# Kernel optimization log

Hardware: AMD Instinct MI355X
Metric: run time of the kernel (lower is better)

## Reference

```python
import jax, jax.numpy as jnp
import numpy as np

S, B, H, N = 512, 32, 512, 131072  # seq_len, batch, hidden_dim, num candidate spans
MAX_STEP = 20  # max_length


def setup_inputs() -> dict:
    key = jax.random.key(0)
    ks = jax.random.split(key, 8)
    hidden = jax.random.normal(ks[0], (S, B, 2 * H), dtype=jnp.float32)
    span_bids = jax.random.randint(ks[1], (N,), 0, B, dtype=jnp.int32)
    # begin in [1, S-1-MAX_STEP-1] so that begin-1>=0 and end=begin+step <= S-1
    span_begins = jax.random.randint(ks[2], (N,), 1, S - MAX_STEP - 2, dtype=jnp.int32)
    steps = jax.random.randint(ks[3], (N,), 2, MAX_STEP + 1, dtype=jnp.int32)
    span_ends = span_begins + steps
    span_flags = jax.random.randint(ks[4], (N,), 0, 2, dtype=jnp.int32)
    span_weights = jax.random.uniform(ks[5], (N,), dtype=jnp.float32)
    W1 = jax.random.normal(ks[6], (2 * H, H), dtype=jnp.float32) / np.sqrt(2.0 * H)
    b1 = jnp.zeros((H,), dtype=jnp.float32)
    W2 = jax.random.normal(ks[7], (H, 1), dtype=jnp.float32) / np.sqrt(float(H))
    b2 = jnp.zeros((1,), dtype=jnp.float32)
    return {"hidden": hidden, "span_bids": span_bids, "span_begins": span_begins,
            "span_ends": span_ends, "span_flags": span_flags, "span_weights": span_weights,
            "W1": W1, "b1": b1, "W2": W2, "b2": b2}


def reference(hidden, span_bids, span_begins, span_ends, span_flags, span_weights, W1, b1, W2, b2):
    h = W2.shape[0]  # hidden_dim
    # vectorized _span_embed: fwd diff on first half, bwd diff on second half
    fwd = hidden[span_ends - 1, span_bids, :h] - hidden[span_begins - 1, span_bids, :h]
    bwd = hidden[span_begins, span_bids, h:] - hidden[span_ends, span_bids, h:]
    feats = jnp.concatenate([fwd, bwd], axis=-1)  # [N, 2H]
    z = jnp.maximum(feats @ W1 + b1, 0.0)
    p = jax.nn.sigmoid(z @ W2 + b2)[:, 0]  # [N]
    targets = (span_flags == 1).astype(p.dtype)
    n_pos = jnp.sum(targets)
    n_tot = jnp.asarray(targets.shape[0], p.dtype)
    scale = 2.0 * n_pos / n_tot  # negative weights scaled by 2*P/(P+N)
    w_eff = jnp.where(span_flags == 1, span_weights, span_weights * scale)
    pc = jnp.clip(p, 1e-7, 1.0 - 1e-7)
    bce = -(targets * jnp.log(pc) + (1.0 - targets) * jnp.log(1.0 - pc))
    loss = jnp.mean(w_eff * bce)
    return loss
```

## Files before the change

kernel.cpp:

```cpp
#include <hip/hip_runtime.h>
#include <hip/hip_bf16.h>


typedef float f32x4 __attribute__((ext_vector_type(4)));
typedef float f32x2 __attribute__((ext_vector_type(2)));
typedef __bf16 bf16x8 __attribute__((ext_vector_type(8)));

__device__ __forceinline__ unsigned short f2bf(float f) {
  unsigned int u = __float_as_uint(f);
  u += 0x7fffu + ((u >> 16) & 1u);
  return (unsigned short)(u >> 16);
}
__device__ __forceinline__ float bf2f(unsigned int lo16) {
  return __uint_as_float(lo16 << 16);
}

__global__ void w1_blocked(const float* __restrict__ W1,
                           unsigned short* __restrict__ W1b) {
  int idx = blockIdx.x * 256 + threadIdx.x;
  int kc = idx & 3;
  int n  = (idx >> 2) & 511;
  int c  = idx >> 11;
  int k0 = c * 32 + kc * 8;
  unsigned short tmp[8];
#pragma unroll
  for (int j = 0; j < 8; ++j)
    tmp[j] = f2bf(W1[(k0 + j) * 512 + n]);
  *(uint4*)(W1b + c * 16384 + n * 32 + kc * 8) = *(uint4*)tmp;
}

__global__ void span_hist(const int* __restrict__ bids, int* __restrict__ ghist,
                          int nspans) {
  __shared__ int h[32];
  int t = threadIdx.x;
  if (t < 32) h[t] = 0;
  __syncthreads();
  int base = blockIdx.x * 1024;
#pragma unroll
  for (int i = 0; i < 4; ++i) {
    int idx = base + t + i * 256;
    if (idx < nspans) atomicAdd(&h[bids[idx]], 1);
  }
  __syncthreads();
  if (t < 32) atomicAdd(&ghist[t], h[t]);
}

__global__ void span_scatter(const int* __restrict__ bids,
                             const int* __restrict__ ghist,
                             int* __restrict__ gslot,
                             int* __restrict__ sidx, int nspans) {
  __shared__ int lh[32], lbase[32], lcur[32];
  int t = threadIdx.x;
  if (t < 32) lh[t] = 0;
  __syncthreads();
  int base = blockIdx.x * 512;
  int myb[2];
#pragma unroll
  for (int i = 0; i < 2; ++i) {
    int idx = base + t + i * 256;
    myb[i] = (idx < nspans) ? bids[idx] : -1;
    if (myb[i] >= 0) atomicAdd(&lh[myb[i]], 1);
  }
  __syncthreads();
  if (t < 32) {
    int pre = 0;
    for (int j = 0; j < t; ++j) pre += ghist[j];
    lbase[t] = pre + atomicAdd(&gslot[t], lh[t]);
    lcur[t] = 0;
  }
  __syncthreads();
#pragma unroll
  for (int i = 0; i < 2; ++i) {
    int b = myb[i];
    if (b >= 0) {
      int pos = lbase[b] + atomicAdd(&lcur[b], 1);
      sidx[pos] = base + t + i * 256;
    }
  }
}

#define APITCH 522
__global__ __launch_bounds__(512, 4) void proj_gemm(
    const float* __restrict__ hidden,
    const unsigned short* __restrict__ w1b,
    unsigned char* __restrict__ Wq) {
  __shared__ __align__(16) unsigned short AH[64 * APITCH];
  unsigned short* Eb = AH;

  const int t = threadIdx.x;
  const int lane = t & 63;
  const int w = t >> 6;
  const int r0 = blockIdx.x << 6;
  const int hk = blockIdx.y << 9;
  const int q = lane >> 4;
  const int m = lane & 15;

  {
    const int col = (t & 31) << 4;
    const int rsub = t >> 5;
#pragma unroll
    for (int p = 0; p < 4; ++p) {
      int row = (p << 4) + rsub;
      const float4* gp = (const float4*)(hidden + ((r0 + row) << 10) + hk + col);
      float4 f0 = gp[0], f1 = gp[1], f2 = gp[2], f3 = gp[3];
      bf16x8 va, vb;
      va[0] = (__bf16)f0.x; va[1] = (__bf16)f0.y;
      va[2] = (__bf16)f0.z; va[3] = (__bf16)f0.w;
      va[4] = (__bf16)f1.x; va[5] = (__bf16)f1.y;
      va[6] = (__bf16)f1.z; va[7] = (__bf16)f1.w;
      vb[0] = (__bf16)f2.x; vb[1] = (__bf16)f2.y;
      vb[2] = (__bf16)f2.z; vb[3] = (__bf16)f2.w;
      vb[4] = (__bf16)f3.x; vb[5] = (__bf16)f3.y;
      vb[6] = (__bf16)f3.z; vb[7] = (__bf16)f3.w;
      unsigned short* dst = AH + row * APITCH + col;
      *(bf16x8*)dst = va;
      *(bf16x8*)(dst + 8) = vb;
    }
  }
  __syncthreads();

  int boffn[4];
#pragma unroll
  for (int nt = 0; nt < 4; ++nt)
    boffn[nt] = (((w << 6) + (nt << 4) + m) << 5) + (q << 3);
  const unsigned short* w1base = w1b + (blockIdx.y << 18);

  f32x4 acc[4][4];
#pragma unroll
  for (int i = 0; i < 4; ++i)
#pragma unroll
    for (int j = 0; j < 4; ++j) acc[i][j] = (f32x4){0.f, 0.f, 0.f, 0.f};

#pragma unroll
  for (int it = 0; it < 16; ++it) {
    const unsigned short* bt = w1base + (it << 14);
    bf16x8 bfr[4];
#pragma unroll
    for (int nt = 0; nt < 4; ++nt)
      bfr[nt] = *(const bf16x8*)(bt + boffn[nt]);
    bf16x8 af[4];
#pragma unroll
    for (int mt = 0; mt < 4; ++mt)
      af[mt] = *(const bf16x8*)(AH + ((mt << 4) + m) * APITCH + (it << 5) + (q << 3));
#pragma unroll
    for (int mt = 0; mt < 4; ++mt)
#pragma unroll
      for (int nt = 0; nt < 4; ++nt)
        acc[mt][nt] = __builtin_amdgcn_mfma_f32_16x16x32_bf16(af[mt], bfr[nt],
                                                              acc[mt][nt], 0, 0, 0);
  }
  __syncthreads();

  unsigned short* Ew = Eb + w * (32 * 72);
#pragma unroll
  for (int pass = 0; pass < 2; ++pass) {
#pragma unroll
    for (int mh = 0; mh < 2; ++mh) {
      int mt = (pass << 1) + mh;
#pragma unroll
      for (int r = 0; r < 4; ++r) {
        int rr = (mh << 4) + ((lane >> 4) << 2) + r;
#pragma unroll
        for (int nt = 0; nt < 4; ++nt)
          Ew[rr * 72 + (nt << 4) + m] = f2bf(acc[mt][nt][r]);
      }
    }
#pragma unroll
    for (int i = 0; i < 4; ++i) {
      int task = (i << 6) + lane;
      int rr = task >> 3;
      int ck = task & 7;
      uint4 v = *(const uint4*)&Ew[rr * 72 + (ck << 3)];
      float f0 = bf2f(v.x & 0xffff), f1 = bf2f(v.x >> 16);
      float f2 = bf2f(v.y & 0xffff), f3 = bf2f(v.y >> 16);
      float f4 = bf2f(v.z & 0xffff), f5 = bf2f(v.z >> 16);
      float f6 = bf2f(v.w & 0xffff), f7 = bf2f(v.w >> 16);
      uint2 o;
      o.x = __builtin_amdgcn_cvt_pk_fp8_f32(f0, f1, 0, false);
      o.x = __builtin_amdgcn_cvt_pk_fp8_f32(f2, f3, o.x, true);
      o.y = __builtin_amdgcn_cvt_pk_fp8_f32(f4, f5, 0, false);
      o.y = __builtin_amdgcn_cvt_pk_fp8_f32(f6, f7, o.y, true);
      int grow = r0 + (pass << 5) + rr;
      int col = (w << 6) + (ck << 3);
      if (hk == 0) {
        *(uint2*)(Wq + (grow << 10) + col) = o;
      } else if (grow >= 32) {
        *(uint2*)(Wq + ((grow - 32) << 10) + 512 + col) = o;
      }
    }
  }
}

#define SPB 64
__global__ __launch_bounds__(256) void span_eval(
    const unsigned char* __restrict__ Wq,
    const int* __restrict__ sidx,
    const int* __restrict__ bids, const int* __restrict__ begins,
    const int* __restrict__ ends, const int* __restrict__ flags,
    const float* __restrict__ weights,
    const float* __restrict__ b1, const float* __restrict__ w2,
    const float* __restrict__ b2, float* __restrict__ partials) {
  __shared__ int oB[SPB], oE[SPB], sfl[SPB];
  __shared__ float swt[SPB];
  __shared__ float red[4][3];
  const int t = threadIdx.x;
  const int lane = t & 63;
  const int w = t >> 6;
  const int h = lane >> 5;
  const int hl = lane & 31;

  const int nblk = gridDim.x;
  int lb = blockIdx.x;
  if ((nblk & 7) == 0) {
    const int cpx = nblk >> 3;
    lb = (blockIdx.x & 7) * cpx + (blockIdx.x >> 3);
  }
  const int sbase = lb * SPB;

  if (t < SPB) {
    int s = sidx[sbase + t];
    int b = bids[s], bg = begins[s], en = ends[s];
    oB[t] = (((bg - 1) << 5) + b) << 10;
    oE[t] = (((en - 1) << 5) + b) << 10;
    sfl[t] = flags[s];
    swt[t] = weights[s];
  }
  __syncthreads();

  const int sp0 = ((w << 1) + h) << 3;
  const int c0 = hl << 4;
  float b1v[16], w2v[16];
#pragma unroll
  for (int q = 0; q < 4; ++q) {
    float4 bv = *(const float4*)(b1 + c0 + (q << 2));
    float4 wv = *(const float4*)(w2 + c0 + (q << 2));
    b1v[(q << 2) + 0] = bv.x; b1v[(q << 2) + 1] = bv.y;
    b1v[(q << 2) + 2] = bv.z; b1v[(q << 2) + 3] = bv.w;
    w2v[(q << 2) + 0] = wv.x; w2v[(q << 2) + 1] = wv.y;
    w2v[(q << 2) + 2] = wv.z; w2v[(q << 2) + 3] = wv.w;
  }

  auto dec = [](unsigned int v, float* f) {
    f32x2 a = __builtin_amdgcn_cvt_pk_f32_fp8(v, false);
    f32x2 b = __builtin_amdgcn_cvt_pk_f32_fp8(v, true);
    f[0] = a[0]; f[1] = a[1]; f[2] = b[0]; f[3] = b[1];
  };

  uint4 BU[3], BV[3], EU[3], EV[3];
  auto ld = [&](int slot, int j) {
    int ob = oB[sp0 + j], oe = oE[sp0 + j];
    BU[slot] = *(const uint4*)(Wq + ob + c0);
    BV[slot] = *(const uint4*)(Wq + ob + 512 + c0);
    EU[slot] = *(const uint4*)(Wq + oe + c0);
    EV[slot] = *(const uint4*)(Wq + oe + 512 + c0);
  };
  ld(0, 0); ld(1, 1); ld(2, 2);

  float mylogit = 0.f;
#pragma unroll
  for (int j = 0; j < 8; ++j) {
    const int slot = j % 3;
    float buf[16], bvf[16], euf[16], evf[16];
    dec(BU[slot].x, buf); dec(BU[slot].y, buf + 4);
    dec(BU[slot].z, buf + 8); dec(BU[slot].w, buf + 12);
    dec(BV[slot].x, bvf); dec(BV[slot].y, bvf + 4);
    dec(BV[slot].z, bvf + 8); dec(BV[slot].w, bvf + 12);
    dec(EU[slot].x, euf); dec(EU[slot].y, euf + 4);
    dec(EU[slot].z, euf + 8); dec(EU[slot].w, euf + 12);
    dec(EV[slot].x, evf); dec(EV[slot].y, evf + 4);
    dec(EV[slot].z, evf + 8); dec(EV[slot].w, evf + 12);
    if (j + 3 < 8) ld(slot, j + 3);
    float sv = 0.f;
#pragma unroll
    for (int k = 0; k < 16; ++k) {
      float zp = euf[k] - buf[k] + bvf[k] - evf[k] + b1v[k];
      sv += fmaxf(zp, 0.f) * w2v[k];
    }
    sv += __shfl_xor(sv, 1);
    sv += __shfl_xor(sv, 2);
    sv += __shfl_xor(sv, 4);
    sv += __shfl_xor(sv, 8);
    sv += __shfl_xor(sv, 16);
    if (hl == j) mylogit = sv;
  }

  mylogit = __shfl(mylogit, ((lane & 8) << 2) + (lane & 7));

  float pos_t = 0.f, neg_t = 0.f, cnt_t = 0.f;
  if (lane < 16) {
    int sl = (w << 4) + lane;
    float logit = mylogit + b2[0];
    float p = 1.f / (1.f + expf(-logit));
    p = fminf(fmaxf(p, 1e-7f), 1.f - 1e-7f);
    int fl = sfl[sl];
    float bce = (fl == 1) ? -logf(p) : -logf(1.f - p);
    float term = swt[sl] * bce;
    pos_t = (fl == 1) ? term : 0.f;
    neg_t = (fl == 1) ? 0.f : term;
    cnt_t = (fl == 1) ? 1.f : 0.f;
  }
#pragma unroll
  for (int off = 1; off < 64; off <<= 1) {
    pos_t += __shfl_xor(pos_t, off);
    neg_t += __shfl_xor(neg_t, off);
    cnt_t += __shfl_xor(cnt_t, off);
  }
  if (lane == 0) { red[w][0] = pos_t; red[w][1] = neg_t; red[w][2] = cnt_t; }
  __syncthreads();
  if (t == 0) {
    partials[(blockIdx.x << 2) + 0] = red[0][0] + red[1][0] + red[2][0] + red[3][0];
    partials[(blockIdx.x << 2) + 1] = red[0][1] + red[1][1] + red[2][1] + red[3][1];
    partials[(blockIdx.x << 2) + 2] = red[0][2] + red[1][2] + red[2][2] + red[3][2];
  }
}

__global__ void finalize(const float* __restrict__ parts, int nblk,
                         float* __restrict__ out, int nspans) {
  __shared__ float sp[4], sn[4], sc[4];
  float P = 0.f, Ng = 0.f, C = 0.f;
  for (int i = threadIdx.x; i < nblk; i += 256) {
    P += parts[(i << 2) + 0];
    Ng += parts[(i << 2) + 1];
    C += parts[(i << 2) + 2];
  }
#pragma unroll
  for (int off = 1; off < 64; off <<= 1) {
    P += __shfl_xor(P, off);
    Ng += __shfl_xor(Ng, off);
    C += __shfl_xor(C, off);
  }
  int w = threadIdx.x >> 6;
  if ((threadIdx.x & 63) == 0) { sp[w] = P; sn[w] = Ng; sc[w] = C; }
  __syncthreads();
  if (threadIdx.x == 0) {
    P = sp[0] + sp[1] + sp[2] + sp[3];
    Ng = sn[0] + sn[1] + sn[2] + sn[3];
    C = sc[0] + sc[1] + sc[2] + sc[3];
    float scale = 2.f * C / (float)nspans;
    out[0] = (P + scale * Ng) / (float)nspans;
  }
}

extern "C" void kernel_launch(void* const* d_in, const int* in_sizes, int n_in,
                              void* d_out, int out_size, void* d_ws, size_t ws_size,
                              hipStream_t stream) {
  const float* hidden = (const float*)d_in[0];
  const int* bids     = (const int*)d_in[1];
  const int* begins   = (const int*)d_in[2];
  const int* ends     = (const int*)d_in[3];
  const int* flags    = (const int*)d_in[4];
  const float* weights = (const float*)d_in[5];
  const float* W1 = (const float*)d_in[6];
  const float* b1 = (const float*)d_in[7];
  const float* W2 = (const float*)d_in[8];
  const float* b2 = (const float*)d_in[9];
  float* out = (float*)d_out;
  const int nspans = in_sizes[1];
  const int nblk = nspans / SPB;

  float* partials = (float*)d_ws;
  unsigned short* W1b = (unsigned short*)((char*)d_ws + (1 << 18));
  unsigned char* Wq = (unsigned char*)((char*)d_ws + (2 << 20));
  int* ghist = (int*)((char*)d_ws + (19 << 20));
  int* gslot = ghist + 32;
  int* sidx  = (int*)((char*)d_ws + (20 << 20));

  hipMemsetAsync(ghist, 0, 64 * sizeof(int), stream);
  w1_blocked<<<256, 256, 0, stream>>>(W1, W1b);
  span_hist<<<(nspans + 1023) / 1024, 256, 0, stream>>>(bids, ghist, nspans);
  span_scatter<<<(nspans + 511) / 512, 256, 0, stream>>>(bids, ghist, gslot,
                                                         sidx, nspans);
  proj_gemm<<<dim3(256, 2), 512, 0, stream>>>(hidden, W1b, Wq);
  span_eval<<<nblk, 256, 0, stream>>>(Wq, sidx, bids, begins, ends, flags,
                                      weights, b1, W2, b2, partials);
  finalize<<<1, 256, 0, stream>>>(partials, nblk, out, nspans);
}
```

Before: 172.0 us.

## Merge prep kernels and retile projection GEMM with swizzled double-chunk LDS staging

Fuses the W1 bf16 blocking kernel and the span histogram kernel into one launch, which saves one launch. Restructures the projection GEMM to use 256-thread blocks over a 3D grid that also splits N, so each block covers 256 output columns. The K dimension is staged through a smaller LDS buffer in two chunks with an XOR-swizzled layout to avoid bank conflicts, and s_setprio is raised around the MFMA blocks. This gives more blocks and smaller LDS for occupancy, but each hidden tile is now loaded and converted twice, once per N half.

```diff
diff --git a/kernel.cpp b/kernel.cpp
--- a/kernel.cpp
+++ b/kernel.cpp
@@ -5,6 +5,7 @@
 typedef float f32x4 __attribute__((ext_vector_type(4)));
 typedef float f32x2 __attribute__((ext_vector_type(2)));
 typedef __bf16 bf16x8 __attribute__((ext_vector_type(8)));
+typedef __bf16 bf16x4 __attribute__((ext_vector_type(4)));
 
 __device__ __forceinline__ unsigned short f2bf(float f) {
   unsigned int u = __float_as_uint(f);
@@ -15,34 +16,35 @@
   return __uint_as_float(lo16 << 16);
 }
 
-__global__ void w1_blocked(const float* __restrict__ W1,
-                           unsigned short* __restrict__ W1b) {
-  int idx = blockIdx.x * 256 + threadIdx.x;
-  int kc = idx & 3;
-  int n  = (idx >> 2) & 511;
-  int c  = idx >> 11;
-  int k0 = c * 32 + kc * 8;
-  unsigned short tmp[8];
-#pragma unroll
-  for (int j = 0; j < 8; ++j)
-    tmp[j] = f2bf(W1[(k0 + j) * 512 + n]);
-  *(uint4*)(W1b + c * 16384 + n * 32 + kc * 8) = *(uint4*)tmp;
-}
-
-__global__ void span_hist(const int* __restrict__ bids, int* __restrict__ ghist,
-                          int nspans) {
+__global__ void prep(const float* __restrict__ W1,
+                     unsigned short* __restrict__ W1b,
+                     const int* __restrict__ bids, int* __restrict__ ghist,
+                     int nspans) {
   __shared__ int h[32];
   int t = threadIdx.x;
-  if (t < 32) h[t] = 0;
-  __syncthreads();
-  int base = blockIdx.x * 1024;
-#pragma unroll
-  for (int i = 0; i < 4; ++i) {
-    int idx = base + t + i * 256;
-    if (idx < nspans) atomicAdd(&h[bids[idx]], 1);
-  }
-  __syncthreads();
-  if (t < 32) atomicAdd(&ghist[t], h[t]);
+  if (blockIdx.x < 256) {
+    int idx = blockIdx.x * 256 + t;
+    int kc = idx & 3;
+    int n  = (idx >> 2) & 511;
+    int c  = idx >> 11;
+    int k0 = c * 32 + kc * 8;
+    unsigned short tmp[8];
+#pragma unroll
+    for (int j = 0; j < 8; ++j)
+      tmp[j] = f2bf(W1[(k0 + j) * 512 + n]);
+    *(uint4*)(W1b + c * 16384 + n * 32 + kc * 8) = *(uint4*)tmp;
+  } else {
+    if (t < 32) h[t] = 0;
+    __syncthreads();
+    int base = (blockIdx.x - 256) * 1024;
+#pragma unroll
+    for (int i = 0; i < 4; ++i) {
+      int idx = base + t + i * 256;
+      if (idx < nspans) atomicAdd(&h[bids[idx]], 1);
+    }
+    __syncthreads();
+    if (t < 32) atomicAdd(&ghist[t], h[t]);
+  }
 }
 
 __global__ void span_scatter(const int* __restrict__ bids,
@@ -79,51 +81,27 @@
   }
 }
 
-#define APITCH 522
-__global__ __launch_bounds__(512, 4) void proj_gemm(
+__global__ __launch_bounds__(256, 4) void proj_gemm(
     const float* __restrict__ hidden,
     const unsigned short* __restrict__ w1b,
     unsigned char* __restrict__ Wq) {
-  __shared__ __align__(16) unsigned short AH[64 * APITCH];
-  unsigned short* Eb = AH;
+  __shared__ __align__(16) unsigned short LB[16384];
 
   const int t = threadIdx.x;
   const int lane = t & 63;
   const int w = t >> 6;
-  const int r0 = blockIdx.x << 6;
-  const int hk = blockIdx.y << 9;
   const int q = lane >> 4;
   const int m = lane & 15;
-
-  {
-    const int col = (t & 31) << 4;
-    const int rsub = t >> 5;
-#pragma unroll
-    for (int p = 0; p < 4; ++p) {
-      int row = (p << 4) + rsub;
-      const float4* gp = (const float4*)(hidden + ((r0 + row) << 10) + hk + col);
-      float4 f0 = gp[0], f1 = gp[1], f2 = gp[2], f3 = gp[3];
-      bf16x8 va, vb;
-      va[0] = (__bf16)f0.x; va[1] = (__bf16)f0.y;
-      va[2] = (__bf16)f0.z; va[3] = (__bf16)f0.w;
-      va[4] = (__bf16)f1.x; va[5] = (__bf16)f1.y;
-      va[6] = (__bf16)f1.z; va[7] = (__bf16)f1.w;
-      vb[0] = (__bf16)f2.x; vb[1] = (__bf16)f2.y;
-      vb[2] = (__bf16)f2.z; vb[3] = (__bf16)f2.w;
-      vb[4] = (__bf16)f3.x; vb[5] = (__bf16)f3.y;
-      vb[6] = (__bf16)f3.z; vb[7] = (__bf16)f3.w;
-      unsigned short* dst = AH + row * APITCH + col;
-      *(bf16x8*)dst = va;
-      *(bf16x8*)(dst + 8) = vb;
-    }
-  }
-  __syncthreads();
-
+  const int r0 = blockIdx.x << 6;
+  const int yc = blockIdx.y << 8;
+  const int z  = blockIdx.z;
+  const int hk = z << 9;
+
+  const unsigned short* w1base = w1b + (z << 18);
   int boffn[4];
 #pragma unroll
   for (int nt = 0; nt < 4; ++nt)
-    boffn[nt] = (((w << 6) + (nt << 4) + m) << 5) + (q << 3);
-  const unsigned short* w1base = w1b + (blockIdx.y << 18);
+    boffn[nt] = ((yc + (w << 6) + (nt << 4) + m) << 5) + (q << 3);
 
   f32x4 acc[4][4];
 #pragma unroll
@@ -131,27 +109,56 @@
 #pragma unroll
     for (int j = 0; j < 4; ++j) acc[i][j] = (f32x4){0.f, 0.f, 0.f, 0.f};
 
-#pragma unroll
-  for (int it = 0; it < 16; ++it) {
-    const unsigned short* bt = w1base + (it << 14);
-    bf16x8 bfr[4];
-#pragma unroll
-    for (int nt = 0; nt < 4; ++nt)
-      bfr[nt] = *(const bf16x8*)(bt + boffn[nt]);
-    bf16x8 af[4];
-#pragma unroll
-    for (int mt = 0; mt < 4; ++mt)
-      af[mt] = *(const bf16x8*)(AH + ((mt << 4) + m) * APITCH + (it << 5) + (q << 3));
-#pragma unroll
-    for (int mt = 0; mt < 4; ++mt)
+  const int s_itL = lane >> 3;
+  const int s_q   = (lane >> 1) & 3;
+  const int s_kk0 = (lane & 1) << 2;
+  const int s_perm = ((s_itL << 1) | (s_itL >> 2)) & 15;
+
+#pragma unroll
+  for (int chunk = 0; chunk < 2; ++chunk) {
+    {
+      const int kb = chunk << 8;
+      const float* gbase = hidden + hk + kb + (lane << 2);
+#pragma unroll
+      for (int i = 0; i < 16; ++i) {
+        int row = (w << 4) + i;
+        float4 f = *(const float4*)(gbase + ((r0 + row) << 10));
+        bf16x4 hv;
+        hv[0] = (__bf16)f.x; hv[1] = (__bf16)f.y;
+        hv[2] = (__bf16)f.z; hv[3] = (__bf16)f.w;
+        int slot = (s_q << 4) + i;
+        int sw = slot ^ s_perm;
+        *(bf16x4*)(LB + (((s_itL << 2) + w) << 9) + (sw << 3) + s_kk0) = hv;
+      }
+    }
+    __syncthreads();
+
+#pragma unroll
+    for (int itL = 0; itL < 8; ++itL) {
+      const unsigned short* bt = w1base + (((chunk << 3) + itL) << 14);
+      bf16x8 bfr[4];
 #pragma unroll
       for (int nt = 0; nt < 4; ++nt)
-        acc[mt][nt] = __builtin_amdgcn_mfma_f32_16x16x32_bf16(af[mt], bfr[nt],
-                                                              acc[mt][nt], 0, 0, 0);
-  }
-  __syncthreads();
-
-  unsigned short* Ew = Eb + w * (32 * 72);
+        bfr[nt] = *(const bf16x8*)(bt + boffn[nt]);
+      const int perm = ((itL << 1) | (itL >> 2)) & 15;
+      const int sw = ((q << 4) + m) ^ perm;
+      bf16x8 af[4];
+#pragma unroll
+      for (int mt = 0; mt < 4; ++mt)
+        af[mt] = *(const bf16x8*)(LB + (((itL << 2) + mt) << 9) + (sw << 3));
+      __builtin_amdgcn_s_setprio(1);
+#pragma unroll
+      for (int mt = 0; mt < 4; ++mt)
+#pragma unroll
+        for (int nt = 0; nt < 4; ++nt)
+          acc[mt][nt] = __builtin_amdgcn_mfma_f32_16x16x32_bf16(af[mt], bfr[nt],
+                                                                acc[mt][nt], 0, 0, 0);
+      __builtin_amdgcn_s_setprio(0);
+    }
+    __syncthreads();
+  }
+
+  unsigned short* Ew = LB + w * (32 * 72);
 #pragma unroll
   for (int pass = 0; pass < 2; ++pass) {
 #pragma unroll
@@ -181,8 +188,8 @@
       o.y = __builtin_amdgcn_cvt_pk_fp8_f32(f4, f5, 0, false);
       o.y = __builtin_amdgcn_cvt_pk_fp8_f32(f6, f7, o.y, true);
       int grow = r0 + (pass << 5) + rr;
-      int col = (w << 6) + (ck << 3);
-      if (hk == 0) {
+      int col = yc + (w << 6) + (ck << 3);
+      if (z == 0) {
         *(uint2*)(Wq + (grow << 10) + col) = o;
       } else if (grow >= 32) {
         *(uint2*)(Wq + ((grow - 32) << 10) + 512 + col) = o;
@@ -231,13 +238,13 @@
   const int c0 = hl << 4;
   float b1v[16], w2v[16];
 #pragma unroll
-  for (int q = 0; q < 4; ++q) {
-    float4 bv = *(const float4*)(b1 + c0 + (q << 2));
-    float4 wv = *(const float4*)(w2 + c0 + (q << 2));
-    b1v[(q << 2) + 0] = bv.x; b1v[(q << 2) + 1] = bv.y;
-    b1v[(q << 2) + 2] = bv.z; b1v[(q << 2) + 3] = bv.w;
-    w2v[(q << 2) + 0] = wv.x; w2v[(q << 2) + 1] = wv.y;
-    w2v[(q << 2) + 2] = wv.z; w2v[(q << 2) + 3] = wv.w;
+  for (int qq = 0; qq < 4; ++qq) {
+    float4 bv = *(const float4*)(b1 + c0 + (qq << 2));
+    float4 wv = *(const float4*)(w2 + c0 + (qq << 2));
+    b1v[(qq << 2) + 0] = bv.x; b1v[(qq << 2) + 1] = bv.y;
+    b1v[(qq << 2) + 2] = bv.z; b1v[(qq << 2) + 3] = bv.w;
+    w2v[(qq << 2) + 0] = wv.x; w2v[(qq << 2) + 1] = wv.y;
+    w2v[(qq << 2) + 2] = wv.z; w2v[(qq << 2) + 3] = wv.w;
   }
 
   auto dec = [](unsigned int v, float* f) {
@@ -366,11 +373,10 @@
   int* sidx  = (int*)((char*)d_ws + (20 << 20));
 
   hipMemsetAsync(ghist, 0, 64 * sizeof(int), stream);
-  w1_blocked<<<256, 256, 0, stream>>>(W1, W1b);
-  span_hist<<<(nspans + 1023) / 1024, 256, 0, stream>>>(bids, ghist, nspans);
+  prep<<<384, 256, 0, stream>>>(W1, W1b, bids, ghist, nspans);
   span_scatter<<<(nspans + 511) / 512, 256, 0, stream>>>(bids, ghist, gslot,
                                                          sidx, nspans);
-  proj_gemm<<<dim3(256, 2), 512, 0, stream>>>(hidden, W1b, Wq);
+  proj_gemm<<<dim3(256, 2, 2), 256, 0, stream>>>(hidden, W1b, Wq);
   span_eval<<<nblk, 256, 0, stream>>>(Wq, sidx, bids, begins, ends, flags,
                                       weights, b1, W2, b2, partials);
   finalize<<<1, 256, 0, stream>>>(partials, nblk, out, nspans);
```

Result: slower. 208.6 us (+21.3%).
